# Optimization experiments

Hardware: AMD Instinct MI355X
Metric: run time of the kernel (lower is better)

Reference implementation:

```python
import jax, jax.numpy as jnp
import numpy as np

N = 100000   # total nodes in batched graph
E = 320000   # total edges
B = 128      # number of graphs in batch
D_IN = 128
H = 256
OUT = 10
L = 4        # num_layers - 1 conv layers
EPS = 1e-6


def setup_inputs() -> dict:
    key = jax.random.key(0)
    ks = jax.random.split(key, 8)
    h = jax.random.normal(ks[0], (N, D_IN), dtype=jnp.float32)
    src = jax.random.randint(ks[1], (E,), 0, N)
    dst = jax.random.randint(ks[2], (E,), 0, N)
    batch_ids = jnp.sort(jax.random.randint(ks[3], (N,), 0, B))
    s = 0.05
    W_first = jax.random.normal(ks[4], (D_IN, H), dtype=jnp.float32) * s
    b_first = jnp.zeros((H,), jnp.float32)
    W_rest = jax.random.normal(ks[5], (L - 1, H, H), dtype=jnp.float32) * s
    b_rest = jnp.zeros((L - 1, H), jnp.float32)
    gamma = jnp.ones((L, H), jnp.float32)
    beta = jnp.zeros((L, H), jnp.float32)
    mean_scale = jnp.ones((L, H), jnp.float32)
    W_pred = jax.random.normal(ks[6], (H, OUT), dtype=jnp.float32) * s
    b_pred = jnp.zeros((OUT,), jnp.float32)
    return dict(h=h, src=src, dst=dst, batch_ids=batch_ids,
                W_first=W_first, b_first=b_first, W_rest=W_rest, b_rest=b_rest,
                gamma=gamma, beta=beta, mean_scale=mean_scale,
                W_pred=W_pred, b_pred=b_pred)


def _graph_conv(h, W, b, src, dst, dinv_src, dinv_dst):
    # DGL GraphConv, norm='both': D_dst^{-1/2} A D_src^{-1/2} h W + b
    x = h * dinv_src[:, None]
    m = jax.ops.segment_sum(x[src], dst, num_segments=N)
    m = m * dinv_dst[:, None]
    return m @ W + b


def _graph_norm(h, gamma, beta, ms, batch_ids, counts):
    # GraphNorm: per-graph mean (scaled by learnable mean_scale) and std
    mean = jax.ops.segment_sum(h, batch_ids, num_segments=B) / counts[:, None]
    sub = h - mean[batch_ids] * ms
    var = jax.ops.segment_sum(sub * sub, batch_ids, num_segments=B) / counts[:, None]
    inv_std = jax.lax.rsqrt(var + EPS)
    return gamma * sub * inv_std[batch_ids] + beta


def reference(h, src, dst, batch_ids, W_first, b_first, W_rest, b_rest,
              gamma, beta, mean_scale, W_pred, b_pred):
    ones_e = jnp.ones((E,), h.dtype)
    deg_out = jnp.maximum(jax.ops.segment_sum(ones_e, src, num_segments=N), 1.0)
    deg_in = jnp.maximum(jax.ops.segment_sum(ones_e, dst, num_segments=N), 1.0)
    dinv_src = jax.lax.rsqrt(deg_out)
    dinv_dst = jax.lax.rsqrt(deg_in)
    counts = jnp.maximum(
        jax.ops.segment_sum(jnp.ones((N,), h.dtype), batch_ids, num_segments=B), 1.0)

    for i in range(L):
        x = h
        if i == 0:
            h = _graph_conv(h, W_first, b_first, src, dst, dinv_src, dinv_dst)
        else:
            h = _graph_conv(h, W_rest[i - 1], b_rest[i - 1], src, dst, dinv_src, dinv_dst)
        h = _graph_norm(h, gamma[i], beta[i], mean_scale[i], batch_ids, counts)
        if i != 0:
            h = jax.nn.relu(h) + x
        else:
            h = jax.nn.relu(h)

    pooled = jax.ops.segment_sum(h, batch_ids, num_segments=B)  # [B, H]
    # dropout is identity at eval
    return pooled @ W_pred + b_pred
```

## Files before the change

### kernel.cpp

```cpp
#include <hip/hip_runtime.h>

#define N_NODES 100000
#define N_PAD   100096
#define N_EDGES 320000
#define NB      128
#define DIN     128
#define H       256
#define OUT_DIM 10
#define EPSV    1e-6f
#define SCAN_B  256
#define PSLICES 32
#define NBLK    (N_PAD / 64)

typedef unsigned short bf16_t;
typedef __attribute__((ext_vector_type(8))) short bf16x8;
typedef __attribute__((ext_vector_type(4))) float f32x4;

__device__ __forceinline__ float bf2f(bf16_t u) {
    union { unsigned int i; float f; } x;
    x.i = ((unsigned int)u) << 16;
    return x.f;
}
__device__ __forceinline__ bf16_t f2bf(float f) {
    union { float f; unsigned int i; } x;
    x.f = f;
    unsigned int r = x.i + 0x7fffu + ((x.i >> 16) & 1u);
    return (bf16_t)(r >> 16);
}

__global__ void k_edge_deg(const int* __restrict__ src, const int* __restrict__ dst,
                           int* deg_out, int* deg_in) {
    int e = blockIdx.x * blockDim.x + threadIdx.x;
    if (e < N_EDGES) {
        atomicAdd(&deg_out[src[e]], 1);
        atomicAdd(&deg_in[dst[e]], 1);
    }
}

__global__ void k_dinv(const int* __restrict__ deg_out, const int* __restrict__ deg_in,
                       float* dinv_src, float* dinv_dst) {
    int n = blockIdx.x * blockDim.x + threadIdx.x;
    if (n < N_NODES) {
        dinv_src[n] = rsqrtf((float)max(deg_out[n], 1));
        dinv_dst[n] = rsqrtf((float)max(deg_in[n], 1));
    }
}

__global__ void k_gstart(const int* __restrict__ bid, int* __restrict__ gstart,
                         float* __restrict__ countsf) {
    int b = threadIdx.x;
    if (b <= NB) {
        int lo = 0, hi = N_NODES;
        while (lo < hi) {
            int mid = (lo + hi) >> 1;
            if (bid[mid] < b) lo = mid + 1; else hi = mid;
        }
        gstart[b] = lo;
    }
    __syncthreads();
    if (b < NB) countsf[b] = (float)max(gstart[b + 1] - gstart[b], 1);
}

__global__ void k_scan1(const int* __restrict__ deg, int* incl, int* bsums) {
    __shared__ int s[SCAN_B];
    int i = blockIdx.x * SCAN_B + threadIdx.x;
    int v = (i < N_NODES) ? deg[i] : 0;
    s[threadIdx.x] = v;
    __syncthreads();
    for (int d = 1; d < SCAN_B; d <<= 1) {
        int t = (threadIdx.x >= d) ? s[threadIdx.x - d] : 0;
        __syncthreads();
        s[threadIdx.x] += t;
        __syncthreads();
    }
    if (i < N_NODES) incl[i] = s[threadIdx.x];
    if (threadIdx.x == SCAN_B - 1) bsums[blockIdx.x] = s[threadIdx.x];
}

__global__ void k_scan2(const int* __restrict__ bsums, int* boffs, int nb) {
    __shared__ int s[512];
    int t = threadIdx.x;
    int v = (t < nb) ? bsums[t] : 0;
    s[t] = v;
    __syncthreads();
    for (int d = 1; d < 512; d <<= 1) {
        int x = (t >= d) ? s[t - d] : 0;
        __syncthreads();
        s[t] += x;
        __syncthreads();
    }
    if (t < nb) boffs[t] = s[t] - v;
}

__global__ void k_scan3(const int* __restrict__ deg, const int* __restrict__ incl,
                        const int* __restrict__ boffs, int* row_start, int* cursor) {
    int i = blockIdx.x * blockDim.x + threadIdx.x;
    if (i < N_NODES) {
        int ex = incl[i] - deg[i] + boffs[i / SCAN_B];
        row_start[i] = ex;
        cursor[i]    = ex;
    }
    if (i == 0) row_start[N_NODES] = N_EDGES;
}

__global__ void k_scatter(const int* __restrict__ src, const int* __restrict__ dst,
                          int* cursor, int* csr_src) {
    int e = blockIdx.x * blockDim.x + threadIdx.x;
    if (e < N_EDGES) {
        int slot = atomicAdd(&cursor[dst[e]], 1);
        csr_src[slot] = src[e];
    }
}

__global__ void k_wt_first(const float* __restrict__ W, bf16_t* __restrict__ Wt) {
    int idx = blockIdx.x * 256 + threadIdx.x;
    if (idx >= H * DIN) return;
    int c = idx / DIN, k = idx % DIN;
    Wt[idx] = f2bf(W[k * H + c]);
}
__global__ void k_wt_rest(const float* __restrict__ W, bf16_t* __restrict__ Wt) {
    int idx = blockIdx.x * 256 + threadIdx.x;
    if (idx >= 3 * H * H) return;
    int l = idx / (H * H);
    int rem = idx % (H * H);
    int c = rem / H, k = rem % H;
    Wt[idx] = f2bf(W[(size_t)l * H * H + k * H + c]);
}

__global__ void k_prescale(const float* __restrict__ h, const float* __restrict__ dinv_s,
                           bf16_t* __restrict__ hs) {
    int idx = blockIdx.x * blockDim.x + threadIdx.x;
    if (idx >= N_NODES * (DIN / 4)) return;
    int n = idx >> 5;
    float w = dinv_s[n];
    float4 v = reinterpret_cast<const float4*>(h)[idx];
    ushort4 o;
    o.x = f2bf(v.x * w); o.y = f2bf(v.y * w);
    o.z = f2bf(v.z * w); o.w = f2bf(v.w * w);
    reinterpret_cast<ushort4*>(hs)[idx] = o;
}

template <int NC, bool PS>
__global__ void k_agg(const bf16_t* __restrict__ hx, const float* __restrict__ dinv_s,
                      const float* __restrict__ dinv_d, const int* __restrict__ row_start,
                      const int* __restrict__ csr_src, bf16_t* __restrict__ m) {
    constexpr int VEC = NC / 64;
    int gid  = blockIdx.x * blockDim.x + threadIdx.x;
    int v    = gid >> 6;
    int lane = gid & 63;
    if (v >= N_NODES) return;
    float acc[VEC] = {};
    int s0 = row_start[v], s1 = row_start[v + 1];

    auto body = [&](int ei) {
        int si = csr_src[ei];
        float wv = 1.f;
        if constexpr (!PS) wv = dinv_s[si];
        if constexpr (VEC == 4) {
            ushort4 r = *reinterpret_cast<const ushort4*>(hx + (size_t)si * NC + lane * 4);
            acc[0] += bf2f(r.x) * wv; acc[1] += bf2f(r.y) * wv;
            acc[2] += bf2f(r.z) * wv; acc[3] += bf2f(r.w) * wv;
        } else {
            ushort2 r = *reinterpret_cast<const ushort2*>(hx + (size_t)si * NC + lane * 2);
            acc[0] += bf2f(r.x) * wv; acc[1] += bf2f(r.y) * wv;
        }
    };

    int e = s0;
    for (; e + 3 < s1; e += 4) { body(e); body(e + 1); body(e + 2); body(e + 3); }
    for (; e < s1; ++e) body(e);

    float wd = dinv_d[v];
    if constexpr (VEC == 4) {
        ushort4 o;
        o.x = f2bf(acc[0] * wd); o.y = f2bf(acc[1] * wd);
        o.z = f2bf(acc[2] * wd); o.w = f2bf(acc[3] * wd);
        *reinterpret_cast<ushort4*>(m + (size_t)v * NC + lane * 4) = o;
    } else {
        ushort2 o; o.x = f2bf(acc[0] * wd); o.y = f2bf(acc[1] * wd);
        *reinterpret_cast<ushort2*>(m + (size_t)v * NC + lane * 2) = o;
    }
}

template <int K>
__global__ __launch_bounds__(256) void k_gemm_mfma(const bf16_t* __restrict__ A,
                                                   const bf16_t* __restrict__ Wt,
                                                   const float* __restrict__ bias,
                                                   const int* __restrict__ bid,
                                                   bf16_t* __restrict__ C,
                                                   float2* __restrict__ part) {
    __shared__ bf16_t lds_raw[64 * (H + 8)];
    __shared__ unsigned char rel_lds[64];
    constexpr int LKA = K + 8;
    bf16_t (*aT)[LKA] = reinterpret_cast<bf16_t (*)[LKA]>(lds_raw);
    bf16_t (*cT)[H + 8] = reinterpret_cast<bf16_t (*)[H + 8]>(lds_raw);

    const int tid  = threadIdx.x;
    const int wave = tid >> 6;
    const int lane = tid & 63;
    const int row0 = blockIdx.x * 64;
    const int col0 = wave * 64;
    const int lr = lane & 15;
    const int lg = lane >> 4;

    {
        const bf16_t* Ag = A + (size_t)row0 * K;
        constexpr int CHUNKS = 64 * K / 8;
        #pragma unroll
        for (int it = 0; it < CHUNKS / 256; ++it) {
            int ci  = it * 256 + tid;
            int row = (ci * 8) / K;
            int col = (ci * 8) % K;
            uint4 v = *reinterpret_cast<const uint4*>(Ag + ci * 8);
            *reinterpret_cast<uint4*>(&aT[row][col]) = v;
        }
    }
    if (tid < 64) {
        int r  = row0 + tid;
        int g0 = bid[(row0 < N_NODES) ? row0 : (N_NODES - 1)];
        rel_lds[tid] = (r < N_NODES) ? (unsigned char)(bid[r] - g0)
                                     : (unsigned char)255;
    }
    __syncthreads();

    f32x4 acc[4][4] = {};

    const bf16_t* Bb = Wt + (size_t)(col0 + lr) * K + lg * 8;

    #pragma unroll
    for (int ks = 0; ks < K / 32; ++ks) {
        bf16x8 a[4], b[4];
        #pragma unroll
        for (int mt = 0; mt < 4; ++mt)
            a[mt] = *reinterpret_cast<const bf16x8*>(&aT[mt * 16 + lr][ks * 32 + lg * 8]);
        #pragma unroll
        for (int nt = 0; nt < 4; ++nt)
            b[nt] = *reinterpret_cast<const bf16x8*>(Bb + (size_t)nt * 16 * K + ks * 32);
        #pragma unroll
        for (int mt = 0; mt < 4; ++mt)
            #pragma unroll
            for (int nt = 0; nt < 4; ++nt)
                acc[mt][nt] = __builtin_amdgcn_mfma_f32_16x16x32_bf16(a[mt], b[nt], acc[mt][nt], 0, 0, 0);
    }

    float bsn[4];
    #pragma unroll
    for (int nt = 0; nt < 4; ++nt) bsn[nt] = bias[col0 + nt * 16 + lr];

    {
        unsigned int relw[4];
        #pragma unroll
        for (int mt = 0; mt < 4; ++mt)
            relw[mt] = *reinterpret_cast<const unsigned int*>(&rel_lds[mt * 16 + lg * 4]);

        float sA[3][4] = {}, qA[3][4] = {};
        #pragma unroll
        for (int mt = 0; mt < 4; ++mt) {
            #pragma unroll
            for (int j = 0; j < 4; ++j) {
                int rv = (relw[mt] >> (8 * j)) & 0xff;
                #pragma unroll
                for (int nt = 0; nt < 4; ++nt) {
                    float v  = acc[mt][nt][j] + bsn[nt];
                    float v0 = (rv == 0) ? v : 0.f;
                    float v1 = (rv == 1) ? v : 0.f;
                    float v2 = (rv == 2) ? v : 0.f;
                    sA[0][nt] += v0; qA[0][nt] += v0 * v0;
                    sA[1][nt] += v1; qA[1][nt] += v1 * v1;
                    sA[2][nt] += v2; qA[2][nt] += v2 * v2;
                }
            }
        }
        #pragma unroll
        for (int rel = 0; rel < 3; ++rel) {
            #pragma unroll
            for (int nt = 0; nt < 4; ++nt) {
                float sv = sA[rel][nt], qv = qA[rel][nt];
                sv += __shfl_xor(sv, 16); qv += __shfl_xor(qv, 16);
                sv += __shfl_xor(sv, 32); qv += __shfl_xor(qv, 32);
                sA[rel][nt] = sv; qA[rel][nt] = qv;
            }
        }
        if (lg == 0) {
            constexpr size_t PLANE = (size_t)NBLK * H;
            #pragma unroll
            for (int rel = 0; rel < 3; ++rel)
                #pragma unroll
                for (int nt = 0; nt < 4; ++nt)
                    part[(size_t)rel * PLANE + (size_t)blockIdx.x * H + col0 + nt * 16 + lr]
                        = make_float2(sA[rel][nt], qA[rel][nt]);
        }
    }

    __syncthreads();

    #pragma unroll
    for (int nt = 0; nt < 4; ++nt) {
        int c = col0 + nt * 16 + lr;
        #pragma unroll
        for (int mt = 0; mt < 4; ++mt) {
            #pragma unroll
            for (int j = 0; j < 4; ++j)
                cT[mt * 16 + lg * 4 + j][c] = f2bf(acc[mt][nt][j] + bsn[nt]);
        }
    }
    __syncthreads();

    #pragma unroll
    for (int it = 0; it < 8; ++it) {
        int i = it * 256 + tid;
        int r = i >> 5;
        int s = i & 31;
        *reinterpret_cast<uint4*>(C + (size_t)(row0 + r) * H + s * 8) =
            *reinterpret_cast<const uint4*>(&cT[r][s * 8]);
    }
}

__global__ void k_stats_red(const float2* __restrict__ part, const int* __restrict__ bid,
                            const int* __restrict__ gstart,
                            float* __restrict__ gsum, float* __restrict__ gsumsq) {
    constexpr size_t PLANE = (size_t)NBLK * H;
    int b = blockIdx.x;
    int c = threadIdx.x;
    int n0 = gstart[b], n1 = gstart[b + 1];
    float s = 0.f, q = 0.f;
    if (n1 > n0) {
        int blo = n0 >> 6, bhi = (n1 - 1) >> 6;
        for (int blk = blo; blk <= bhi; ++blk) {
            int rel = b - bid[blk << 6];
            if (rel >= 0 && rel < 3) {
                float2 v = part[(size_t)rel * PLANE + (size_t)blk * H + c];
                s += v.x; q += v.y;
            }
        }
    }
    gsum[b * H + c]   = s;
    gsumsq[b * H + c] = q;
}

template <bool RES>
__global__ void k_norm(const bf16_t* __restrict__ y, const bf16_t* __restrict__ resid,
                       const int* __restrict__ bid, const float* __restrict__ gsum,
                       const float* __restrict__ gsumsq, const float* __restrict__ countsf,
                       const float* __restrict__ gamma, const float* __restrict__ beta,
                       const float* __restrict__ msc, bf16_t* __restrict__ outp) {
    int idx = blockIdx.x * blockDim.x + threadIdx.x;
    if (idx >= N_NODES * (H / 4)) return;
    int n  = idx >> 6;
    int f4 = idx & 63;
    int b  = bid[n];
    float rc = 1.0f / countsf[b];
    float4 s4  = reinterpret_cast<const float4*>(gsum)[b * 64 + f4];
    float4 q4  = reinterpret_cast<const float4*>(gsumsq)[b * 64 + f4];
    float4 g4  = reinterpret_cast<const float4*>(gamma)[f4];
    float4 be4 = reinterpret_cast<const float4*>(beta)[f4];
    float4 m4  = reinterpret_cast<const float4*>(msc)[f4];
    ushort4 yv = reinterpret_cast<const ushort4*>(y)[idx];

    auto nrm = [&](float s, float q, float ga, float be, float m, float yy) {
        float mean = s * rc, ex2 = q * rc;
        float mm   = mean * m;
        float var  = ex2 - 2.f * mean * mm + mm * mm;
        float a    = ga * rsqrtf(var + EPSV);
        return fmaxf(yy * a + (be - a * mm), 0.f);
    };
    float o0 = nrm(s4.x, q4.x, g4.x, be4.x, m4.x, bf2f(yv.x));
    float o1 = nrm(s4.y, q4.y, g4.y, be4.y, m4.y, bf2f(yv.y));
    float o2 = nrm(s4.z, q4.z, g4.z, be4.z, m4.z, bf2f(yv.z));
    float o3 = nrm(s4.w, q4.w, g4.w, be4.w, m4.w, bf2f(yv.w));
    if constexpr (RES) {
        ushort4 r = reinterpret_cast<const ushort4*>(resid)[idx];
        o0 += bf2f(r.x); o1 += bf2f(r.y); o2 += bf2f(r.z); o3 += bf2f(r.w);
    }
    ushort4 o;
    o.x = f2bf(o0); o.y = f2bf(o1); o.z = f2bf(o2); o.w = f2bf(o3);
    reinterpret_cast<ushort4*>(outp)[idx] = o;
}

__global__ void k_pool(const bf16_t* __restrict__ hf, const int* __restrict__ gstart,
                       float* pooled) {
    int b = blockIdx.x, sl = blockIdx.y, f = threadIdx.x;
    int n0 = gstart[b], n1 = gstart[b + 1];
    int cnt = n1 - n0;
    int lo = n0 + (int)((long long)cnt * sl / PSLICES);
    int hi = n0 + (int)((long long)cnt * (sl + 1) / PSLICES);
    if (lo >= hi) return;
    float s = 0.f;
    for (int n = lo; n < hi; ++n) s += bf2f(hf[(size_t)n * H + f]);
    atomicAdd(&pooled[b * H + f], s);
}

__global__ void k_pred(const float* __restrict__ pooled, const float* __restrict__ Wp,
                       const float* __restrict__ bp, float* __restrict__ outp) {
    __shared__ float row[H];
    int b = blockIdx.x;
    row[threadIdx.x] = pooled[b * H + threadIdx.x];
    __syncthreads();
    if (threadIdx.x < OUT_DIM) {
        float acc = bp[threadIdx.x];
        for (int f = 0; f < H; ++f) acc += row[f] * Wp[f * OUT_DIM + threadIdx.x];
        outp[b * OUT_DIM + threadIdx.x] = acc;
    }
}

extern "C" void kernel_launch(void* const* d_in, const int* in_sizes, int n_in,
                              void* d_out, int out_size, void* d_ws, size_t ws_size,
                              hipStream_t stream) {
    const float* h_in  = (const float*)d_in[0];
    const int*   src   = (const int*)d_in[1];
    const int*   dst   = (const int*)d_in[2];
    const int*   bid   = (const int*)d_in[3];
    const float* Wf    = (const float*)d_in[4];
    const float* bfv   = (const float*)d_in[5];
    const float* Wr    = (const float*)d_in[6];
    const float* br    = (const float*)d_in[7];
    const float* gamma = (const float*)d_in[8];
    const float* beta  = (const float*)d_in[9];
    const float* ms    = (const float*)d_in[10];
    const float* Wp    = (const float*)d_in[11];
    const float* bp    = (const float*)d_in[12];
    float* outp = (float*)d_out;

    char* w = (char*)d_ws;
    size_t off = 0;
    auto alloc = [&](size_t bytes) -> void* {
        void* p = w + off;
        off = (off + bytes + 255) & ~(size_t)255;
        return p;
    };
    bf16_t* bufA = (bf16_t*)alloc((size_t)N_PAD * H * 2);
    bf16_t* bufB = (bf16_t*)alloc((size_t)N_PAD * H * 2);
    bf16_t* bufC = (bf16_t*)alloc((size_t)N_PAD * H * 2);
    bf16_t* Wt0  = (bf16_t*)alloc((size_t)H * DIN * 2);
    bf16_t* Wt123= (bf16_t*)alloc((size_t)3 * H * H * 2);
    int* deg_out_i = (int*)alloc(N_NODES * 4);
    int* deg_in_i  = (int*)alloc(N_NODES * 4);
    float* dinv_src = (float*)alloc(N_NODES * 4);
    float* dinv_dst = (float*)alloc(N_NODES * 4);
    int* incl_tmp  = (int*)alloc(N_NODES * 4);
    int* bsums     = (int*)alloc(512 * 4);
    int* boffs     = (int*)alloc(512 * 4);
    int* row_start = (int*)alloc((N_NODES + 1) * 4);
    int* cursor    = (int*)alloc(N_NODES * 4);
    int* csr_src   = (int*)alloc(N_EDGES * 4);
    int* gstart    = (int*)alloc((NB + 1) * 4);
    float* countsf = (float*)alloc(NB * 4);
    float* gsum    = (float*)alloc((size_t)NB * H * 4);
    float* gsumsq  = (float*)alloc((size_t)NB * H * 4);
    float2* part   = (float2*)alloc((size_t)3 * NBLK * H * 8);
    float* pooled  = (float*)alloc(NB * H * 4);

    if (off > ws_size) return;

    bf16_t* hs = bufB;

    const int nscan = (N_NODES + SCAN_B - 1) / SCAN_B;

    hipMemsetAsync(deg_out_i, 0, N_NODES * 4, stream);
    hipMemsetAsync(deg_in_i, 0, N_NODES * 4, stream);
    hipMemsetAsync(pooled, 0, NB * H * 4, stream);

    k_edge_deg<<<(N_EDGES + 255) / 256, 256, 0, stream>>>(src, dst, deg_out_i, deg_in_i);
    k_gstart<<<1, 256, 0, stream>>>(bid, gstart, countsf);
    k_dinv<<<(N_NODES + 255) / 256, 256, 0, stream>>>(deg_out_i, deg_in_i, dinv_src, dinv_dst);
    k_scan1<<<nscan, SCAN_B, 0, stream>>>(deg_in_i, incl_tmp, bsums);
    k_scan2<<<1, 512, 0, stream>>>(bsums, boffs, nscan);
    k_scan3<<<(N_NODES + 255) / 256, 256, 0, stream>>>(deg_in_i, incl_tmp, boffs, row_start, cursor);
    k_scatter<<<(N_EDGES + 255) / 256, 256, 0, stream>>>(src, dst, cursor, csr_src);
    k_wt_first<<<(H * DIN + 255) / 256, 256, 0, stream>>>(Wf, Wt0);
    k_wt_rest<<<(3 * H * H + 255) / 256, 256, 0, stream>>>(Wr, Wt123);

    const int aggGrid  = (N_NODES + 3) / 4;
    const int normGrid = (N_NODES * (H / 4) + 255) / 256;
    const int gemmGrid = NBLK;

    k_prescale<<<(N_NODES * (DIN / 4) + 255) / 256, 256, 0, stream>>>(h_in, dinv_src, hs);
    k_agg<DIN, true><<<aggGrid, 256, 0, stream>>>(hs, nullptr, dinv_dst, row_start, csr_src, bufA);
    k_gemm_mfma<DIN><<<gemmGrid, 256, 0, stream>>>(bufA, Wt0, bfv, bid, bufB, part);
    k_stats_red<<<NB, H, 0, stream>>>(part, bid, gstart, gsum, gsumsq);
    k_norm<false><<<normGrid, 256, 0, stream>>>(bufB, nullptr, bid, gsum, gsumsq, countsf,
                                                gamma, beta, ms, bufC);

    bf16_t* hx = bufC;
    bf16_t* f1 = bufA;
    bf16_t* f2 = bufB;
    for (int i = 1; i < 4; ++i) {
        k_agg<H, false><<<aggGrid, 256, 0, stream>>>(hx, dinv_src, dinv_dst, row_start, csr_src, f1);
        k_gemm_mfma<H><<<gemmGrid, 256, 0, stream>>>(f1, Wt123 + (size_t)(i - 1) * H * H,
                                                     br + (i - 1) * H, bid, f2, part);
        k_stats_red<<<NB, H, 0, stream>>>(part, bid, gstart, gsum, gsumsq);
        k_norm<true><<<normGrid, 256, 0, stream>>>(f2, hx, bid, gsum, gsumsq, countsf,
                                                   gamma + i * H, beta + i * H, ms + i * H, f1);
        bf16_t* nh = f1; f1 = hx; hx = nh;
    }

    k_pool<<<dim3(NB, PSLICES), H, 0, stream>>>(hx, gstart, pooled);
    k_pred<<<NB, H, 0, stream>>>(pooled, Wp, bp, outp);
}
```

Baseline: 594.3 us.

## Double-buffer GEMM A tiles via direct global-to-LDS loads, two tiles per block

The GEMM kernel now handles two 64-row tiles per block and uses two LDS buffers. While one tile is computed, the next A tile is prefetched with global_load_lds, using an XOR-swizzled layout to avoid bank conflicts. Per-tile graph-relative ids are precomputed once into a packed array, so the GEMM no longer reads batch_ids. This halves the grid and doubles LDS use per block, which can lower occupancy and parallelism on a large-CU GPU.

Result: slower. 665.1 us (+11.9%).

```diff
diff --git a/kernel.cpp b/kernel.cpp
--- a/kernel.cpp
+++ b/kernel.cpp
@@ -11,6 +11,7 @@
 #define SCAN_B  256
 #define PSLICES 32
 #define NBLK    (N_PAD / 64)
+#define GEMM_G  (NBLK / 2)
 
 typedef unsigned short bf16_t;
 typedef __attribute__((ext_vector_type(8))) short bf16x8;
@@ -26,6 +27,13 @@
     x.f = f;
     unsigned int r = x.i + 0x7fffu + ((x.i >> 16) & 1u);
     return (bf16_t)(r >> 16);
+}
+
+__device__ __forceinline__ void load_lds16(const bf16_t* g, bf16_t* l) {
+    __builtin_amdgcn_global_load_lds(
+        (const __attribute__((address_space(1))) unsigned int*)g,
+        (__attribute__((address_space(3))) unsigned int*)l,
+        16, 0, 0);
 }
 
 __global__ void k_edge_deg(const int* __restrict__ src, const int* __restrict__ dst,
@@ -59,6 +67,25 @@
     }
     __syncthreads();
     if (b < NB) countsf[b] = (float)max(gstart[b + 1] - gstart[b], 1);
+}
+
+__global__ void k_relpk(const int* __restrict__ bid, unsigned int* __restrict__ relpk) {
+    int idx = blockIdx.x * blockDim.x + threadIdx.x;
+    if (idx >= NBLK * 16) return;
+    int t = idx >> 4, w = idx & 15;
+    int row0 = t * 64;
+    int g0 = bid[(row0 < N_NODES) ? row0 : (N_NODES - 1)];
+    unsigned int pk = 0;
+    for (int j = 0; j < 4; ++j) {
+        int r = row0 + w * 4 + j;
+        unsigned int rel = 255u;
+        if (r < N_NODES) {
+            int d = bid[r] - g0;
+            rel = (d >= 0 && d < 255) ? (unsigned int)d : 255u;
+        }
+        pk |= rel << (8 * j);
+    }
+    relpk[idx] = pk;
 }
 
 __global__ void k_scan1(const int* __restrict__ deg, int* incl, int* bsums) {
@@ -186,133 +213,143 @@
 __global__ __launch_bounds__(256) void k_gemm_mfma(const bf16_t* __restrict__ A,
                                                    const bf16_t* __restrict__ Wt,
                                                    const float* __restrict__ bias,
-                                                   const int* __restrict__ bid,
+                                                   const unsigned int* __restrict__ relpk,
                                                    bf16_t* __restrict__ C,
                                                    float2* __restrict__ part) {
-    __shared__ bf16_t lds_raw[64 * (H + 8)];
-    __shared__ unsigned char rel_lds[64];
-    constexpr int LKA = K + 8;
-    bf16_t (*aT)[LKA] = reinterpret_cast<bf16_t (*)[LKA]>(lds_raw);
-    bf16_t (*cT)[H + 8] = reinterpret_cast<bf16_t (*)[H + 8]>(lds_raw);
+    __shared__ bf16_t lds0[64 * (H + 8)];
+    __shared__ bf16_t lds1[64 * (H + 8)];
+
+    constexpr int CPR   = K / 8;
+    constexpr int ITERS = CPR / 4;
 
     const int tid  = threadIdx.x;
     const int wave = tid >> 6;
     const int lane = tid & 63;
-    const int row0 = blockIdx.x * 64;
     const int col0 = wave * 64;
     const int lr = lane & 15;
     const int lg = lane >> 4;
 
-    {
-        const bf16_t* Ag = A + (size_t)row0 * K;
-        constexpr int CHUNKS = 64 * K / 8;
-        #pragma unroll
-        for (int it = 0; it < CHUNKS / 256; ++it) {
-            int ci  = it * 256 + tid;
-            int row = (ci * 8) / K;
-            int col = (ci * 8) % K;
-            uint4 v = *reinterpret_cast<const uint4*>(Ag + ci * 8);
-            *reinterpret_cast<uint4*>(&aT[row][col]) = v;
-        }
-    }
-    if (tid < 64) {
-        int r  = row0 + tid;
-        int g0 = bid[(row0 < N_NODES) ? row0 : (N_NODES - 1)];
-        rel_lds[tid] = (r < N_NODES) ? (unsigned char)(bid[r] - g0)
-                                     : (unsigned char)255;
-    }
-    __syncthreads();
-
-    f32x4 acc[4][4] = {};
-
-    const bf16_t* Bb = Wt + (size_t)(col0 + lr) * K + lg * 8;
-
-    #pragma unroll
-    for (int ks = 0; ks < K / 32; ++ks) {
-        bf16x8 a[4], b[4];
-        #pragma unroll
-        for (int mt = 0; mt < 4; ++mt)
-            a[mt] = *reinterpret_cast<const bf16x8*>(&aT[mt * 16 + lr][ks * 32 + lg * 8]);
-        #pragma unroll
-        for (int nt = 0; nt < 4; ++nt)
-            b[nt] = *reinterpret_cast<const bf16x8*>(Bb + (size_t)nt * 16 * K + ks * 32);
-        #pragma unroll
-        for (int mt = 0; mt < 4; ++mt)
-            #pragma unroll
-            for (int nt = 0; nt < 4; ++nt)
-                acc[mt][nt] = __builtin_amdgcn_mfma_f32_16x16x32_bf16(a[mt], b[nt], acc[mt][nt], 0, 0, 0);
-    }
-
     float bsn[4];
     #pragma unroll
     for (int nt = 0; nt < 4; ++nt) bsn[nt] = bias[col0 + nt * 16 + lr];
 
-    {
+    const bf16_t* Bb = Wt + (size_t)(col0 + lr) * K + lg * 8;
+
+    auto STAGE = [&](bf16_t* buf, int tile) {
+        const bf16_t* Ag = A + (size_t)tile * 64 * K;
+        #pragma unroll
+        for (int it = 0; it < ITERS; ++it) {
+            int wb  = it * 256 + wave * 64;
+            int L   = wb + lane;
+            int row = L / CPR;
+            int c16 = L % CPR;
+            const bf16_t* gp = Ag + row * K + ((c16 ^ (row & 7)) << 3);
+            load_lds16(gp, buf + (size_t)wb * 8);
+        }
+    };
+
+    const int t0 = blockIdx.x;
+    STAGE(lds0, t0);
+
+    int cur = 0;
+    #pragma unroll
+    for (int ti = 0; ti < 2; ++ti) {
+        const int tile = t0 + ti * GEMM_G;
+        bf16_t* bufc = cur ? lds1 : lds0;
+        bf16_t* bufn = cur ? lds0 : lds1;
+
+        __syncthreads();
+        if (ti + 1 < 2) STAGE(bufn, tile + GEMM_G);
+
         unsigned int relw[4];
         #pragma unroll
         for (int mt = 0; mt < 4; ++mt)
-            relw[mt] = *reinterpret_cast<const unsigned int*>(&rel_lds[mt * 16 + lg * 4]);
-
-        float sA[3][4] = {}, qA[3][4] = {};
+            relw[mt] = relpk[tile * 16 + mt * 4 + lg];
+
+        f32x4 acc[4][4] = {};
+
         #pragma unroll
-        for (int mt = 0; mt < 4; ++mt) {
+        for (int ks = 0; ks < K / 32; ++ks) {
+            bf16x8 a[4], b[4];
+            const int sw = ((ks * 4 + lg) ^ (lr & 7)) << 3;
             #pragma unroll
-            for (int j = 0; j < 4; ++j) {
-                int rv = (relw[mt] >> (8 * j)) & 0xff;
+            for (int mt = 0; mt < 4; ++mt)
+                a[mt] = *reinterpret_cast<const bf16x8*>(bufc + (mt * 16 + lr) * K + sw);
+            #pragma unroll
+            for (int nt = 0; nt < 4; ++nt)
+                b[nt] = *reinterpret_cast<const bf16x8*>(Bb + (size_t)nt * 16 * K + ks * 32);
+            #pragma unroll
+            for (int mt = 0; mt < 4; ++mt)
+                #pragma unroll
+                for (int nt = 0; nt < 4; ++nt)
+                    acc[mt][nt] = __builtin_amdgcn_mfma_f32_16x16x32_bf16(a[mt], b[nt], acc[mt][nt], 0, 0, 0);
+        }
+
+        {
+            float sA[3][4] = {}, qA[3][4] = {};
+            #pragma unroll
+            for (int mt = 0; mt < 4; ++mt) {
+                #pragma unroll
+                for (int j = 0; j < 4; ++j) {
+                    int rv = (relw[mt] >> (8 * j)) & 0xff;
+                    #pragma unroll
+                    for (int nt = 0; nt < 4; ++nt) {
+                        float v  = acc[mt][nt][j] + bsn[nt];
+                        float v0 = (rv == 0) ? v : 0.f;
+                        float v1 = (rv == 1) ? v : 0.f;
+                        float v2 = (rv == 2) ? v : 0.f;
+                        sA[0][nt] += v0; qA[0][nt] += v0 * v0;
+                        sA[1][nt] += v1; qA[1][nt] += v1 * v1;
+                        sA[2][nt] += v2; qA[2][nt] += v2 * v2;
+                    }
+                }
+            }
+            #pragma unroll
+            for (int rel = 0; rel < 3; ++rel) {
                 #pragma unroll
                 for (int nt = 0; nt < 4; ++nt) {
-                    float v  = acc[mt][nt][j] + bsn[nt];
-                    float v0 = (rv == 0) ? v : 0.f;
-                    float v1 = (rv == 1) ? v : 0.f;
-                    float v2 = (rv == 2) ? v : 0.f;
-                    sA[0][nt] += v0; qA[0][nt] += v0 * v0;
-                    sA[1][nt] += v1; qA[1][nt] += v1 * v1;
-                    sA[2][nt] += v2; qA[2][nt] += v2 * v2;
+                    float sv = sA[rel][nt], qv = qA[rel][nt];
+                    sv += __shfl_xor(sv, 16); qv += __shfl_xor(qv, 16);
+                    sv += __shfl_xor(sv, 32); qv += __shfl_xor(qv, 32);
+                    sA[rel][nt] = sv; qA[rel][nt] = qv;
                 }
             }
-        }
+            if (lg == 0) {
+                constexpr size_t PLANE = (size_t)NBLK * H;
+                #pragma unroll
+                for (int rel = 0; rel < 3; ++rel)
+                    #pragma unroll
+                    for (int nt = 0; nt < 4; ++nt)
+                        part[(size_t)rel * PLANE + (size_t)tile * H + col0 + nt * 16 + lr]
+                            = make_float2(sA[rel][nt], qA[rel][nt]);
+            }
+        }
+
+        __syncthreads();
+
+        bf16_t (*cT)[H + 8] = reinterpret_cast<bf16_t (*)[H + 8]>(bufc);
         #pragma unroll
-        for (int rel = 0; rel < 3; ++rel) {
+        for (int nt = 0; nt < 4; ++nt) {
+            int c = col0 + nt * 16 + lr;
             #pragma unroll
-            for (int nt = 0; nt < 4; ++nt) {
-                float sv = sA[rel][nt], qv = qA[rel][nt];
-                sv += __shfl_xor(sv, 16); qv += __shfl_xor(qv, 16);
-                sv += __shfl_xor(sv, 32); qv += __shfl_xor(qv, 32);
-                sA[rel][nt] = sv; qA[rel][nt] = qv;
+            for (int mt = 0; mt < 4; ++mt) {
+                #pragma unroll
+                for (int j = 0; j < 4; ++j)
+                    cT[mt * 16 + lg * 4 + j][c] = f2bf(acc[mt][nt][j] + bsn[nt]);
             }
         }
-        if (lg == 0) {
-            constexpr size_t PLANE = (size_t)NBLK * H;
-            #pragma unroll
-            for (int rel = 0; rel < 3; ++rel)
-                #pragma unroll
-                for (int nt = 0; nt < 4; ++nt)
-                    part[(size_t)rel * PLANE + (size_t)blockIdx.x * H + col0 + nt * 16 + lr]
-                        = make_float2(sA[rel][nt], qA[rel][nt]);
-        }
-    }
-
-    __syncthreads();
-
-    #pragma unroll
-    for (int nt = 0; nt < 4; ++nt) {
-        int c = col0 + nt * 16 + lr;
+        __syncthreads();
+
+        const int row0 = tile * 64;
         #pragma unroll
-        for (int mt = 0; mt < 4; ++mt) {
-            #pragma unroll
-            for (int j = 0; j < 4; ++j)
-                cT[mt * 16 + lg * 4 + j][c] = f2bf(acc[mt][nt][j] + bsn[nt]);
-        }
-    }
-    __syncthreads();
-
-    #pragma unroll
-    for (int it = 0; it < 8; ++it) {
-        int i = it * 256 + tid;
-        int r = i >> 5;
-        int s = i & 31;
-        *reinterpret_cast<uint4*>(C + (size_t)(row0 + r) * H + s * 8) =
-            *reinterpret_cast<const uint4*>(&cT[r][s * 8]);
+        for (int it = 0; it < 8; ++it) {
+            int i = it * 256 + tid;
+            int r = i >> 5;
+            int s = i & 31;
+            *reinterpret_cast<uint4*>(C + (size_t)(row0 + r) * H + s * 8) =
+                *reinterpret_cast<const uint4*>(&cT[r][s * 8]);
+        }
+        cur ^= 1;
     }
 }
 
@@ -448,6 +485,7 @@
     float* gsum    = (float*)alloc((size_t)NB * H * 4);
     float* gsumsq  = (float*)alloc((size_t)NB * H * 4);
     float2* part   = (float2*)alloc((size_t)3 * NBLK * H * 8);
+    unsigned int* relpk = (unsigned int*)alloc((size_t)NBLK * 16 * 4);
     float* pooled  = (float*)alloc(NB * H * 4);
 
     if (off > ws_size) return;
@@ -462,6 +500,7 @@
 
     k_edge_deg<<<(N_EDGES + 255) / 256, 256, 0, stream>>>(src, dst, deg_out_i, deg_in_i);
     k_gstart<<<1, 256, 0, stream>>>(bid, gstart, countsf);
+    k_relpk<<<(NBLK * 16 + 255) / 256, 256, 0, stream>>>(bid, relpk);
     k_dinv<<<(N_NODES + 255) / 256, 256, 0, stream>>>(deg_out_i, deg_in_i, dinv_src, dinv_dst);
     k_scan1<<<nscan, SCAN_B, 0, stream>>>(deg_in_i, incl_tmp, bsums);
     k_scan2<<<1, 512, 0, stream>>>(bsums, boffs, nscan);
@@ -472,11 +511,10 @@
 
     const int aggGrid  = (N_NODES + 3) / 4;
     const int normGrid = (N_NODES * (H / 4) + 255) / 256;
-    const int gemmGrid = NBLK;
 
     k_prescale<<<(N_NODES * (DIN / 4) + 255) / 256, 256, 0, stream>>>(h_in, dinv_src, hs);
     k_agg<DIN, true><<<aggGrid, 256, 0, stream>>>(hs, nullptr, dinv_dst, row_start, csr_src, bufA);
-    k_gemm_mfma<DIN><<<gemmGrid, 256, 0, stream>>>(bufA, Wt0, bfv, bid, bufB, part);
+    k_gemm_mfma<DIN><<<GEMM_G, 256, 0, stream>>>(bufA, Wt0, bfv, relpk, bufB, part);
     k_stats_red<<<NB, H, 0, stream>>>(part, bid, gstart, gsum, gsumsq);
     k_norm<false><<<normGrid, 256, 0, stream>>>(bufB, nullptr, bid, gsum, gsumsq, countsf,
                                                 gamma, beta, ms, bufC);
@@ -486,8 +524,8 @@
     bf16_t* f2 = bufB;
     for (int i = 1; i < 4; ++i) {
         k_agg<H, false><<<aggGrid, 256, 0, stream>>>(hx, dinv_src, dinv_dst, row_start, csr_src, f1);
-        k_gemm_mfma<H><<<gemmGrid, 256, 0, stream>>>(f1, Wt123 + (size_t)(i - 1) * H * H,
-                                                     br + (i - 1) * H, bid, f2, part);
+        k_gemm_mfma<H><<<GEMM_G, 256, 0, stream>>>(f1, Wt123 + (size_t)(i - 1) * H * H,
+                                                   br + (i - 1) * H, relpk, f2, part);
         k_stats_red<<<NB, H, 0, stream>>>(part, bid, gstart, gsum, gsumsq);
         k_norm<true><<<normGrid, 256, 0, stream>>>(f2, hx, bid, gsum, gsumsq, countsf,
                                                    gamma + i * H, beta + i * H, ms + i * H, f1);
```

## Halve GEMM row tile to 32 and precompute packed graph-relative ids

Applied to the files above, without the earlier changes.

Shrinks the MFMA GEMM row tile from 64 to 32 rows, which doubles the block count (about 3128 blocks) and halves LDS per block, aiming for better occupancy and load balance across CUs. The per-row graph-relative ids are now computed once by a new kernel into a packed buffer, removing the per-block bid loads and the LDS staging plus barrier for them. The trade-off is that each block reuses the W tile over fewer rows, so weight reads from cache go up and the partial-stats buffer doubles, which also gives the stats reduction more blocks to scan.

After: 659.9 us. +11.0%, slower.

```diff
diff --git a/kernel.cpp b/kernel.cpp
--- a/kernel.cpp
+++ b/kernel.cpp
@@ -10,7 +10,7 @@
 #define EPSV    1e-6f
 #define SCAN_B  256
 #define PSLICES 32
-#define NBLK    (N_PAD / 64)
+#define NBLK32  (N_PAD / 32)
 
 typedef unsigned short bf16_t;
 typedef __attribute__((ext_vector_type(8))) short bf16x8;
@@ -59,6 +59,25 @@
     }
     __syncthreads();
     if (b < NB) countsf[b] = (float)max(gstart[b + 1] - gstart[b], 1);
+}
+
+__global__ void k_relpk(const int* __restrict__ bid, unsigned int* __restrict__ relpk) {
+    int idx = blockIdx.x * blockDim.x + threadIdx.x;
+    if (idx >= NBLK32 * 8) return;
+    int t = idx >> 3, w = idx & 7;
+    int row0 = t * 32;
+    int g0 = bid[(row0 < N_NODES) ? row0 : (N_NODES - 1)];
+    unsigned int pk = 0;
+    for (int j = 0; j < 4; ++j) {
+        int r = row0 + w * 4 + j;
+        unsigned int rel = 255u;
+        if (r < N_NODES) {
+            int d = bid[r] - g0;
+            rel = (d >= 0 && d < 255) ? (unsigned int)d : 255u;
+        }
+        pk |= rel << (8 * j);
+    }
+    relpk[idx] = pk;
 }
 
 __global__ void k_scan1(const int* __restrict__ deg, int* incl, int* bsums) {
@@ -186,11 +205,10 @@
 __global__ __launch_bounds__(256) void k_gemm_mfma(const bf16_t* __restrict__ A,
                                                    const bf16_t* __restrict__ Wt,
                                                    const float* __restrict__ bias,
-                                                   const int* __restrict__ bid,
+                                                   const unsigned int* __restrict__ relpk,
                                                    bf16_t* __restrict__ C,
                                                    float2* __restrict__ part) {
-    __shared__ bf16_t lds_raw[64 * (H + 8)];
-    __shared__ unsigned char rel_lds[64];
+    __shared__ bf16_t lds_raw[32 * (H + 8)];
     constexpr int LKA = K + 8;
     bf16_t (*aT)[LKA] = reinterpret_cast<bf16_t (*)[LKA]>(lds_raw);
     bf16_t (*cT)[H + 8] = reinterpret_cast<bf16_t (*)[H + 8]>(lds_raw);
@@ -198,14 +216,14 @@
     const int tid  = threadIdx.x;
     const int wave = tid >> 6;
     const int lane = tid & 63;
-    const int row0 = blockIdx.x * 64;
+    const int row0 = blockIdx.x * 32;
     const int col0 = wave * 64;
     const int lr = lane & 15;
     const int lg = lane >> 4;
 
     {
         const bf16_t* Ag = A + (size_t)row0 * K;
-        constexpr int CHUNKS = 64 * K / 8;
+        constexpr int CHUNKS = 32 * K / 8;
         #pragma unroll
         for (int it = 0; it < CHUNKS / 256; ++it) {
             int ci  = it * 256 + tid;
@@ -215,29 +233,23 @@
             *reinterpret_cast<uint4*>(&aT[row][col]) = v;
         }
     }
-    if (tid < 64) {
-        int r  = row0 + tid;
-        int g0 = bid[(row0 < N_NODES) ? row0 : (N_NODES - 1)];
-        rel_lds[tid] = (r < N_NODES) ? (unsigned char)(bid[r] - g0)
-                                     : (unsigned char)255;
-    }
-    __syncthreads();
-
-    f32x4 acc[4][4] = {};
+    __syncthreads();
+
+    f32x4 acc[2][4] = {};
 
     const bf16_t* Bb = Wt + (size_t)(col0 + lr) * K + lg * 8;
 
     #pragma unroll
     for (int ks = 0; ks < K / 32; ++ks) {
-        bf16x8 a[4], b[4];
-        #pragma unroll
-        for (int mt = 0; mt < 4; ++mt)
+        bf16x8 a[2], b[4];
+        #pragma unroll
+        for (int mt = 0; mt < 2; ++mt)
             a[mt] = *reinterpret_cast<const bf16x8*>(&aT[mt * 16 + lr][ks * 32 + lg * 8]);
         #pragma unroll
         for (int nt = 0; nt < 4; ++nt)
             b[nt] = *reinterpret_cast<const bf16x8*>(Bb + (size_t)nt * 16 * K + ks * 32);
         #pragma unroll
-        for (int mt = 0; mt < 4; ++mt)
+        for (int mt = 0; mt < 2; ++mt)
             #pragma unroll
             for (int nt = 0; nt < 4; ++nt)
                 acc[mt][nt] = __builtin_amdgcn_mfma_f32_16x16x32_bf16(a[mt], b[nt], acc[mt][nt], 0, 0, 0);
@@ -248,14 +260,14 @@
     for (int nt = 0; nt < 4; ++nt) bsn[nt] = bias[col0 + nt * 16 + lr];
 
     {
-        unsigned int relw[4];
-        #pragma unroll
-        for (int mt = 0; mt < 4; ++mt)
-            relw[mt] = *reinterpret_cast<const unsigned int*>(&rel_lds[mt * 16 + lg * 4]);
+        unsigned int relw[2];
+        #pragma unroll
+        for (int mt = 0; mt < 2; ++mt)
+            relw[mt] = relpk[blockIdx.x * 8 + mt * 4 + lg];
 
         float sA[3][4] = {}, qA[3][4] = {};
         #pragma unroll
-        for (int mt = 0; mt < 4; ++mt) {
+        for (int mt = 0; mt < 2; ++mt) {
             #pragma unroll
             for (int j = 0; j < 4; ++j) {
                 int rv = (relw[mt] >> (8 * j)) & 0xff;
@@ -282,7 +294,7 @@
             }
         }
         if (lg == 0) {
-            constexpr size_t PLANE = (size_t)NBLK * H;
+            constexpr size_t PLANE = (size_t)NBLK32 * H;
             #pragma unroll
             for (int rel = 0; rel < 3; ++rel)
                 #pragma unroll
@@ -298,7 +310,7 @@
     for (int nt = 0; nt < 4; ++nt) {
         int c = col0 + nt * 16 + lr;
         #pragma unroll
-        for (int mt = 0; mt < 4; ++mt) {
+        for (int mt = 0; mt < 2; ++mt) {
             #pragma unroll
             for (int j = 0; j < 4; ++j)
                 cT[mt * 16 + lg * 4 + j][c] = f2bf(acc[mt][nt][j] + bsn[nt]);
@@ -307,7 +319,7 @@
     __syncthreads();
 
     #pragma unroll
-    for (int it = 0; it < 8; ++it) {
+    for (int it = 0; it < 4; ++it) {
         int i = it * 256 + tid;
         int r = i >> 5;
         int s = i & 31;
@@ -319,15 +331,15 @@
 __global__ void k_stats_red(const float2* __restrict__ part, const int* __restrict__ bid,
                             const int* __restrict__ gstart,
                             float* __restrict__ gsum, float* __restrict__ gsumsq) {
-    constexpr size_t PLANE = (size_t)NBLK * H;
+    constexpr size_t PLANE = (size_t)NBLK32 * H;
     int b = blockIdx.x;
     int c = threadIdx.x;
     int n0 = gstart[b], n1 = gstart[b + 1];
     float s = 0.f, q = 0.f;
     if (n1 > n0) {
-        int blo = n0 >> 6, bhi = (n1 - 1) >> 6;
+        int blo = n0 >> 5, bhi = (n1 - 1) >> 5;
         for (int blk = blo; blk <= bhi; ++blk) {
-            int rel = b - bid[blk << 6];
+            int rel = b - bid[blk << 5];
             if (rel >= 0 && rel < 3) {
                 float2 v = part[(size_t)rel * PLANE + (size_t)blk * H + c];
                 s += v.x; q += v.y;
@@ -447,7 +459,8 @@
     float* countsf = (float*)alloc(NB * 4);
     float* gsum    = (float*)alloc((size_t)NB * H * 4);
     float* gsumsq  = (float*)alloc((size_t)NB * H * 4);
-    float2* part   = (float2*)alloc((size_t)3 * NBLK * H * 8);
+    float2* part   = (float2*)alloc((size_t)3 * NBLK32 * H * 8);
+    unsigned int* relpk = (unsigned int*)alloc((size_t)NBLK32 * 8 * 4);
     float* pooled  = (float*)alloc(NB * H * 4);
 
     if (off > ws_size) return;
@@ -462,6 +475,7 @@
 
     k_edge_deg<<<(N_EDGES + 255) / 256, 256, 0, stream>>>(src, dst, deg_out_i, deg_in_i);
     k_gstart<<<1, 256, 0, stream>>>(bid, gstart, countsf);
+    k_relpk<<<(NBLK32 * 8 + 255) / 256, 256, 0, stream>>>(bid, relpk);
     k_dinv<<<(N_NODES + 255) / 256, 256, 0, stream>>>(deg_out_i, deg_in_i, dinv_src, dinv_dst);
     k_scan1<<<nscan, SCAN_B, 0, stream>>>(deg_in_i, incl_tmp, bsums);
     k_scan2<<<1, 512, 0, stream>>>(bsums, boffs, nscan);
@@ -472,11 +486,10 @@
 
     const int aggGrid  = (N_NODES + 3) / 4;
     const int normGrid = (N_NODES * (H / 4) + 255) / 256;
-    const int gemmGrid = NBLK;
 
     k_prescale<<<(N_NODES * (DIN / 4) + 255) / 256, 256, 0, stream>>>(h_in, dinv_src, hs);
     k_agg<DIN, true><<<aggGrid, 256, 0, stream>>>(hs, nullptr, dinv_dst, row_start, csr_src, bufA);
-    k_gemm_mfma<DIN><<<gemmGrid, 256, 0, stream>>>(bufA, Wt0, bfv, bid, bufB, part);
+    k_gemm_mfma<DIN><<<NBLK32, 256, 0, stream>>>(bufA, Wt0, bfv, relpk, bufB, part);
     k_stats_red<<<NB, H, 0, stream>>>(part, bid, gstart, gsum, gsumsq);
     k_norm<false><<<normGrid, 256, 0, stream>>>(bufB, nullptr, bid, gsum, gsumsq, countsf,
                                                 gamma, beta, ms, bufC);
@@ -486,8 +499,8 @@
     bf16_t* f2 = bufB;
     for (int i = 1; i < 4; ++i) {
         k_agg<H, false><<<aggGrid, 256, 0, stream>>>(hx, dinv_src, dinv_dst, row_start, csr_src, f1);
-        k_gemm_mfma<H><<<gemmGrid, 256, 0, stream>>>(f1, Wt123 + (size_t)(i - 1) * H * H,
-                                                     br + (i - 1) * H, bid, f2, part);
+        k_gemm_mfma<H><<<NBLK32, 256, 0, stream>>>(f1, Wt123 + (size_t)(i - 1) * H * H,
+                                                   br + (i - 1) * H, relpk, f2, part);
         k_stats_red<<<NB, H, 0, stream>>>(part, bid, gstart, gsum, gsumsq);
         k_norm<true><<<normGrid, 256, 0, stream>>>(f2, hx, bid, gsum, gsumsq, countsf,
                                                    gamma + i * H, beta + i * H, ms + i * H, f1);
```
